# Optimization experiments

Measured on AMD Instinct MI355X. Metric: run time of the kernel, lower is better.

## Reference

```python
import jax, jax.numpy as jnp
import numpy as np

B, T, C, H = 2, 2048, 1024, 16  # batch, seq (== block_size), n_embd, n_head
HD = C // H  # head dim


def setup_inputs() -> dict:
    key = jax.random.key(0)
    k1, k2, k3 = jax.random.split(key, 3)
    x = jax.random.normal(k1, (B, T, C), dtype=jnp.float32)
    w_attn = jax.random.normal(k2, (C, 3 * C), dtype=jnp.float32) * (1.0 / np.sqrt(C))
    b_attn = jnp.zeros((3 * C,), dtype=jnp.float32)
    w_proj = jax.random.normal(k3, (C, C), dtype=jnp.float32) * (1.0 / np.sqrt(C))
    b_proj = jnp.zeros((C,), dtype=jnp.float32)
    return {"x": x, "w_attn": w_attn, "b_attn": b_attn, "w_proj": w_proj, "b_proj": b_proj}


def reference(x, w_attn, b_attn, w_proj, b_proj):
    # qkv projection: [B,T,3C]
    qkv = x @ w_attn + b_attn
    q, k, v = jnp.split(qkv, 3, axis=-1)
    # -> [B,H,T,HD]
    def to_heads(t):
        return t.reshape(B, T, H, HD).transpose(0, 2, 1, 3)
    q, k, v = to_heads(q), to_heads(k), to_heads(v)
    scale = 1.0 / np.sqrt(HD).astype(np.float32)
    # att: [B,H,T,T]
    att = jnp.einsum("bhqd,bhkd->bhqk", q, k) * scale
    causal = jnp.tril(jnp.ones((T, T), dtype=bool))
    att = jnp.where(causal[None, None], att, -jnp.inf)
    att = jax.nn.softmax(att, axis=-1)
    # y: [B,H,T,HD] -> [B,T,C]
    y = jnp.einsum("bhqk,bhkd->bhqd", att, v)
    y = y.transpose(0, 2, 1, 3).reshape(B, T, C)
    return y @ w_proj + b_proj
```

## Files before the change

kernel.cpp:

```cpp
#include <hip/hip_runtime.h>
#include <stdint.h>

#define Bb 2
#define Tt 2048
#define Cc 1024
#define Hh 16
#define HD 64
#define C3 3072

typedef __bf16 bf16x8 __attribute__((ext_vector_type(8)));
typedef float  f32x4  __attribute__((ext_vector_type(4)));
typedef unsigned short u16;
typedef u16 u16x8 __attribute__((ext_vector_type(8)));
typedef u16 u16x4 __attribute__((ext_vector_type(4)));

#define SCALE2 0.18033688f

__device__ __forceinline__ u16 f2bf(float f) {
  union { float f; unsigned u; } v; v.f = f;
  return (u16)((v.u + 0x7fffu + ((v.u >> 16) & 1u)) >> 16);
}
__device__ __forceinline__ u16 f2bf_fast(float f) {
  union { float f; unsigned u; } v; v.f = f;
  return (u16)((v.u + 0x8000u) >> 16);
}
__device__ __forceinline__ float bf2f(u16 a) {
  union { unsigned u; float f; } v; v.u = ((unsigned)a) << 16; return v.f;
}

__device__ __forceinline__ void gl2lds16(const void* g, void* s) {
  __builtin_amdgcn_global_load_lds(
      (__attribute__((address_space(1))) void*)(g),
      (__attribute__((address_space(3))) void*)(s), 16, 0, 0);
}

__device__ __forceinline__ bf16x8 ldb8(const u16* p) {
  return __builtin_bit_cast(bf16x8, *(const u16x8*)p);
}

__global__ __launch_bounds__(256)
void prep_kernel(const float* __restrict__ x, const float* __restrict__ w_attn,
                 const float* __restrict__ w_proj, u16* __restrict__ xb,
                 u16* __restrict__ wat, u16* __restrict__ wpt) {
  __shared__ u16 tile[64][65];
  const int blk = blockIdx.x;
  const int tid = threadIdx.x;
  if (blk < 4096) {
    int i = blk * 256 + tid;
    float4 v = ((const float4*)x)[i];
    u16x4 o = { f2bf(v.x), f2bf(v.y), f2bf(v.z), f2bf(v.w) };
    ((u16x4*)xb)[i] = o;
    return;
  }
  const float* in; u16* out; int R, C, c0, r0;
  if (blk < 4096 + 768) {
    int t = blk - 4096;
    in = w_attn; out = wat; R = 1024; C = 3072;
    c0 = (t % 48) * 64; r0 = (t / 48) * 64;
  } else {
    int t = blk - 4864;
    in = w_proj; out = wpt; R = 1024; C = 1024;
    c0 = (t & 15) * 64; r0 = (t >> 4) * 64;
  }
  int xx = tid & 63, yy = tid >> 6;
  #pragma unroll
  for (int rr = yy; rr < 64; rr += 4)
    tile[rr][xx] = f2bf(in[(size_t)(r0 + rr) * C + c0 + xx]);
  __syncthreads();
  #pragma unroll
  for (int rr = yy; rr < 64; rr += 4)
    out[(size_t)(c0 + rr) * R + r0 + xx] = tile[xx][rr];
}

template <int MODE, int BN>
__global__ __launch_bounds__(256, 4)
void gemm_bt(const u16* __restrict__ A, const u16* __restrict__ Bt,
             const float* __restrict__ bias, void* __restrict__ Cout,
             u16* __restrict__ Vt, int M, int N, int K) {
  __shared__ u16 As[2][128 * 32];
  __shared__ u16 Bs[2][BN * 32];
  constexpr int JT = BN / 32;
  const int tid = threadIdx.x;
  const int ln  = tid & 63;
  const int w   = tid >> 6;
  const int wm  = w >> 1, wn = w & 1;
  const int l15 = ln & 15, lq = ln >> 4;
  const int swz2 = (l15 >> 1) & 3;
  const int m0 = blockIdx.y * 128, n0 = blockIdx.x * BN;

  int aoff[2], boff[BN / 128 + 1];
  #pragma unroll
  for (int i = 0; i < 2; ++i) {
    int s = i * 256 + tid;
    int row = s >> 2, cg = (s & 3) ^ ((s >> 3) & 3);
    aoff[i] = (m0 + row) * K + cg * 8;
  }
  #pragma unroll
  for (int i = 0; i < BN / 128 + 1; ++i) {
    int s = i * 256 + tid;
    int row = s >> 2, cg = (s & 3) ^ ((s >> 3) & 3);
    boff[i] = (n0 + row) * K + cg * 8;
  }

  f32x4 acc[4][JT];
  #pragma unroll
  for (int i = 0; i < 4; ++i)
    #pragma unroll
    for (int j = 0; j < JT; ++j)
      acc[i][j] = (f32x4){0.f, 0.f, 0.f, 0.f};

  const int NK = K >> 5;
  #pragma unroll
  for (int i = 0; i < 2; ++i)
    gl2lds16(A + aoff[i], (char*)As[0] + (size_t)(i * 256 + w * 64) * 16);
  #pragma unroll
  for (int i = 0; i < BN / 128 + 1; ++i)
    gl2lds16(Bt + boff[i], (char*)Bs[0] + (size_t)(i * 256 + w * 64) * 16);

  for (int it = 0; it < NK; ++it) {
    const int p = it & 1;
    __syncthreads();
    if (it + 1 < NK) {
      const int k0 = (it + 1) * 32;
      #pragma unroll
      for (int i = 0; i < 2; ++i)
        gl2lds16(A + aoff[i] + k0, (char*)As[p ^ 1] + (size_t)(i * 256 + w * 64) * 16);
      #pragma unroll
      for (int i = 0; i < BN / 128 + 1; ++i)
        gl2lds16(Bt + boff[i] + k0, (char*)Bs[p ^ 1] + (size_t)(i * 256 + w * 64) * 16);
    }
    const u16* AsB = As[p];
    const u16* BsB = Bs[p];
    bf16x8 af[4], bfr[JT];
    #pragma unroll
    for (int i = 0; i < 4; ++i)
      af[i] = ldb8(&AsB[(wm * 64 + i * 16 + l15) * 32 + ((lq ^ swz2) * 8)]);
    #pragma unroll
    for (int j = 0; j < JT; ++j)
      bfr[j] = ldb8(&BsB[(wn * (BN / 2) + j * 16 + l15) * 32 + ((lq ^ swz2) * 8)]);
    #pragma unroll
    for (int i = 0; i < 4; ++i)
      #pragma unroll
      for (int j = 0; j < JT; ++j)
        acc[i][j] = __builtin_amdgcn_mfma_f32_16x16x32_bf16(af[i], bfr[j], acc[i][j], 0, 0, 0);
  }

  if (MODE == 1 && n0 >= 2048) {
    #pragma unroll
    for (int i = 0; i < 4; ++i) {
      int rowb = m0 + wm * 64 + i * 16 + lq * 4;
      int b_ = rowb >> 11, t0 = rowb & 2047;
      int tl = t0 & 63;
      int c = tl >> 4, ll = (tl >> 2) & 3;
      int pos0 = (c >> 1) * 32 + ll * 8 + (c & 1) * 4;
      size_t tdst = (size_t)(t0 & ~63) + pos0;
      #pragma unroll
      for (int j = 0; j < JT; ++j) {
        int col = n0 + wn * (BN / 2) + j * 16 + l15;
        int hd = col - 2048;
        float bsv = bias[col];
        u16x4 pk;
        #pragma unroll
        for (int r = 0; r < 4; ++r) pk[r] = f2bf(acc[i][j][r] + bsv);
        *(u16x4*)&Vt[(size_t)(b_ * 1024 + hd) * Tt + tdst] = pk;
      }
    }
  } else {
    const int ldc = (MODE == 1) ? 2048 : N;
    #pragma unroll
    for (int i = 0; i < 4; ++i) {
      int row = m0 + wm * 64 + i * 16 + lq * 4;
      #pragma unroll
      for (int j = 0; j < JT; ++j) {
        int col = n0 + wn * (BN / 2) + j * 16 + l15;
        float bsv = bias[col];
        #pragma unroll
        for (int r = 0; r < 4; ++r) {
          float v = acc[i][j][r] + bsv;
          if (MODE == 1) ((u16*)Cout)[(size_t)(row + r) * ldc + col] = f2bf(v);
          else           ((float*)Cout)[(size_t)(row + r) * ldc + col] = v;
        }
      }
    }
  }
}


__device__ __forceinline__ bf16x8 packp(const f32x4& a, const f32x4& b) {
  u16x8 u = { f2bf_fast(a[0]), f2bf_fast(a[1]), f2bf_fast(a[2]), f2bf_fast(a[3]),
              f2bf_fast(b[0]), f2bf_fast(b[1]), f2bf_fast(b[2]), f2bf_fast(b[3]) };
  return __builtin_bit_cast(bf16x8, u);
}
__device__ __forceinline__ bf16x8 qscale(const u16* p) {
  u16x8 q = *(const u16x8*)p;
  u16x8 s;
  #pragma unroll
  for (int j = 0; j < 8; ++j) s[j] = f2bf(bf2f(q[j]) * SCALE2);
  return __builtin_bit_cast(bf16x8, s);
}

__global__ __launch_bounds__(256, 4)
void attn_fused(const u16* __restrict__ qk, const u16* __restrict__ vt,
                u16* __restrict__ y) {
  __shared__ u16 Ks[2][64 * 64];
  __shared__ u16 Vts[2][64 * 64];
  const int tid = threadIdx.x;
  const int ln = tid & 63, w = tid >> 6;
  const int l15 = ln & 15, lq = ln >> 4;
  const int swz = l15 & 7;
  const int bx = blockIdx.x;
  const int bh = bx & 31;
  const int h  = bh & 15, b = bh >> 4;
  const int rr_ = bx >> 8, g = (bx >> 5) & 7;
  const int qt = (rr_ == 0) ? 31 - g : (rr_ == 1) ? 16 + g : (rr_ == 2) ? 15 - g : g;
  const int q0 = qt * 64;
  const int q0w = q0 + w * 16;

  const u16* qbase = qk + (size_t)(b * Tt) * 2048 + h * HD;
  const u16* kbase = qk + (size_t)(b * Tt) * 2048 + 1024 + h * HD;
  const u16* vbase = vt + (size_t)(b * 1024 + h * HD) * Tt;

  const int s0 = tid, s1 = 256 + tid;
  const int koff0 = (s0 >> 3) * 2048 + (((s0 & 7) ^ ((s0 >> 3) & 7)) * 8);
  const int koff1 = (s1 >> 3) * 2048 + (((s1 & 7) ^ ((s1 >> 3) & 7)) * 8);

  const u16* qrA = qbase + (size_t)(q0w + l15) * 2048;
  bf16x8 qA0 = qscale(qrA + lq * 8), qA1 = qscale(qrA + 32 + lq * 8);

  f32x4 o[4];
  #pragma unroll
  for (int j = 0; j < 4; ++j) o[j] = (f32x4){0,0,0,0};
  float m = -__builtin_inff(), l = 0.f;
  const int qg = q0w + l15;

  const int nkv = qt + 1;

  {
    gl2lds16(kbase + koff0, (char*)Ks[0] + w * 1024);
    gl2lds16(kbase + koff1, (char*)Ks[0] + 4096 + w * 1024);
    gl2lds16(vbase + koff0, (char*)Vts[0] + w * 1024);
    gl2lds16(vbase + koff1, (char*)Vts[0] + 4096 + w * 1024);
  }

  for (int it = 0; it < nkv; ++it) {
    const int kk = it * 64;
    const int p = it & 1;
    __syncthreads();
    if (it + 1 < nkv) {
      const u16* ksrc = kbase + (size_t)(kk + 64) * 2048;
      const u16* vsrc = vbase + kk + 64;
      gl2lds16(ksrc + koff0, (char*)Ks[p ^ 1] + w * 1024);
      gl2lds16(ksrc + koff1, (char*)Ks[p ^ 1] + 4096 + w * 1024);
      gl2lds16(vsrc + koff0, (char*)Vts[p ^ 1] + w * 1024);
      gl2lds16(vsrc + koff1, (char*)Vts[p ^ 1] + 4096 + w * 1024);
    }
    const u16* KsB  = Ks[p];
    const u16* VtsB = Vts[p];

    f32x4 t[4];
    #pragma unroll
    for (int i = 0; i < 4; ++i) t[i] = (f32x4){0,0,0,0};
    #pragma unroll
    for (int i = 0; i < 4; ++i) {
      bf16x8 kf0 = ldb8(&KsB[(i * 16 + l15) * 64 + ((lq    ) ^ swz) * 8]);
      bf16x8 kf1 = ldb8(&KsB[(i * 16 + l15) * 64 + ((lq + 4) ^ swz) * 8]);
      t[i] = __builtin_amdgcn_mfma_f32_16x16x32_bf16(kf0, qA0, t[i], 0, 0, 0);
      t[i] = __builtin_amdgcn_mfma_f32_16x16x32_bf16(kf1, qA1, t[i], 0, 0, 0);
    }

    const bool lastI = (it == nkv - 1);
    if (lastI) {
      #pragma unroll
      for (int i = 0; i < 4; ++i)
        #pragma unroll
        for (int r = 0; r < 4; ++r) {
          int kv = kk + i * 16 + lq * 4 + r;
          if (kv > qg) t[i][r] = -__builtin_inff();
        }
    }
    float mx = t[0][0];
    #pragma unroll
    for (int i = 0; i < 4; ++i)
      #pragma unroll
      for (int r = 0; r < 4; ++r) mx = fmaxf(mx, t[i][r]);
    mx = fmaxf(mx, __shfl_xor(mx, 16));
    mx = fmaxf(mx, __shfl_xor(mx, 32));
    float mn = fmaxf(m, mx);
    float al = __builtin_amdgcn_exp2f(m - mn);
    float ps = 0.f;
    #pragma unroll
    for (int i = 0; i < 4; ++i)
      #pragma unroll
      for (int r = 0; r < 4; ++r) {
        float pp = __builtin_amdgcn_exp2f(t[i][r] - mn);
        t[i][r] = pp;
        ps += pp;
      }
    ps += __shfl_xor(ps, 16);
    ps += __shfl_xor(ps, 32);
    l = l * al + ps;
    m = mn;
    #pragma unroll
    for (int jd = 0; jd < 4; ++jd)
      #pragma unroll
      for (int r = 0; r < 4; ++r) o[jd][r] *= al;

    bf16x8 p0 = packp(t[0], t[1]), p1 = packp(t[2], t[3]);
    #pragma unroll
    for (int mf = 0; mf < 2; ++mf) {
      bf16x8 pb = mf ? p1 : p0;
      #pragma unroll
      for (int jd = 0; jd < 4; ++jd) {
        int d = jd * 16 + l15;
        bf16x8 vf = ldb8(&VtsB[d * 64 + ((mf * 4 + lq) ^ swz) * 8]);
        o[jd] = __builtin_amdgcn_mfma_f32_16x16x32_bf16(vf, pb, o[jd], 0, 0, 0);
      }
    }
  }

  float inv = 1.f / l;
  const size_t ybase = (size_t)(b * Tt + q0w + l15) * Cc + h * HD;
  #pragma unroll
  for (int jd = 0; jd < 4; ++jd) {
    u16x4 pk;
    #pragma unroll
    for (int r = 0; r < 4; ++r) pk[r] = f2bf(o[jd][r] * inv);
    *(u16x4*)&y[ybase + jd * 16 + lq * 4] = pk;
  }
}

extern "C" void kernel_launch(void* const* d_in, const int* in_sizes, int n_in,
                              void* d_out, int out_size, void* d_ws, size_t ws_size,
                              hipStream_t stream) {
  const float* x      = (const float*)d_in[0];
  const float* w_attn = (const float*)d_in[1];
  const float* b_attn = (const float*)d_in[2];
  const float* w_proj = (const float*)d_in[3];
  const float* b_proj = (const float*)d_in[4];
  float* out = (float*)d_out;

  char* ws = (char*)d_ws;
  u16* xb  = (u16*)(ws + 0);
  u16* wat = (u16*)(ws + 8388608);
  u16* wpt = (u16*)(ws + 14680064);
  u16* qkb = (u16*)(ws + 16777216);
  u16* vtb = (u16*)(ws + 33554432);
  u16* yb  = (u16*)(ws + 41943040);

  prep_kernel<<<5120, 256, 0, stream>>>(x, w_attn, w_proj, xb, wat, wpt);
  gemm_bt<1, 128><<<dim3(24, 32), 256, 0, stream>>>(xb, wat, b_attn, (void*)qkb, vtb, 4096, 3072, 1024);
  attn_fused<<<1024, 256, 0, stream>>>(qkb, vtb, yb);
  gemm_bt<0, 64><<<dim3(16, 32), 256, 0, stream>>>(yb, wpt, b_proj, (void*)out, nullptr, 4096, 1024, 1024);
}
```

Baseline: 181.5 us.

## Pair complementary causal query tiles per block and add lazy softmax rescaling

Each attention block now processes two query tiles, qt and 31-qt, one after the other, so every block does the same number of KV iterations. Grid size drops from 1024 to 512, and the KV double buffer is prefetched across the boundary between the two tiles. The softmax rescale of the output accumulator is skipped unless the running max grows by more than a threshold, the P matrix is packed with native bf16 conversion, and the MFMA sections get raised wave priority. The trade-off is fewer blocks to hide latency, longer dependent work per block, and extra control flow.

```diff
diff --git a/kernel.cpp b/kernel.cpp
--- a/kernel.cpp
+++ b/kernel.cpp
@@ -19,10 +19,6 @@
 __device__ __forceinline__ u16 f2bf(float f) {
   union { float f; unsigned u; } v; v.f = f;
   return (u16)((v.u + 0x7fffu + ((v.u >> 16) & 1u)) >> 16);
-}
-__device__ __forceinline__ u16 f2bf_fast(float f) {
-  union { float f; unsigned u; } v; v.f = f;
-  return (u16)((v.u + 0x8000u) >> 16);
 }
 __device__ __forceinline__ float bf2f(u16 a) {
   union { unsigned u; float f; } v; v.u = ((unsigned)a) << 16; return v.f;
@@ -187,9 +183,10 @@
 
 
 __device__ __forceinline__ bf16x8 packp(const f32x4& a, const f32x4& b) {
-  u16x8 u = { f2bf_fast(a[0]), f2bf_fast(a[1]), f2bf_fast(a[2]), f2bf_fast(a[3]),
-              f2bf_fast(b[0]), f2bf_fast(b[1]), f2bf_fast(b[2]), f2bf_fast(b[3]) };
-  return __builtin_bit_cast(bf16x8, u);
+  bf16x8 r;
+  #pragma unroll
+  for (int i = 0; i < 4; ++i) { r[i] = (__bf16)a[i]; r[i + 4] = (__bf16)b[i]; }
+  return r;
 }
 __device__ __forceinline__ bf16x8 qscale(const u16* p) {
   u16x8 q = *(const u16x8*)p;
@@ -211,10 +208,7 @@
   const int bx = blockIdx.x;
   const int bh = bx & 31;
   const int h  = bh & 15, b = bh >> 4;
-  const int rr_ = bx >> 8, g = (bx >> 5) & 7;
-  const int qt = (rr_ == 0) ? 31 - g : (rr_ == 1) ? 16 + g : (rr_ == 2) ? 15 - g : g;
-  const int q0 = qt * 64;
-  const int q0w = q0 + w * 16;
+  const int pr = bx >> 5;
 
   const u16* qbase = qk + (size_t)(b * Tt) * 2048 + h * HD;
   const u16* kbase = qk + (size_t)(b * Tt) * 2048 + 1024 + h * HD;
@@ -224,108 +218,130 @@
   const int koff0 = (s0 >> 3) * 2048 + (((s0 & 7) ^ ((s0 >> 3) & 7)) * 8);
   const int koff1 = (s1 >> 3) * 2048 + (((s1 & 7) ^ ((s1 >> 3) & 7)) * 8);
 
-  const u16* qrA = qbase + (size_t)(q0w + l15) * 2048;
-  bf16x8 qA0 = qscale(qrA + lq * 8), qA1 = qscale(qrA + 32 + lq * 8);
-
-  f32x4 o[4];
-  #pragma unroll
-  for (int j = 0; j < 4; ++j) o[j] = (f32x4){0,0,0,0};
-  float m = -__builtin_inff(), l = 0.f;
-  const int qg = q0w + l15;
-
-  const int nkv = qt + 1;
-
-  {
-    gl2lds16(kbase + koff0, (char*)Ks[0] + w * 1024);
-    gl2lds16(kbase + koff1, (char*)Ks[0] + 4096 + w * 1024);
-    gl2lds16(vbase + koff0, (char*)Vts[0] + w * 1024);
-    gl2lds16(vbase + koff1, (char*)Vts[0] + 4096 + w * 1024);
-  }
-
-  for (int it = 0; it < nkv; ++it) {
-    const int kk = it * 64;
-    const int p = it & 1;
-    __syncthreads();
-    if (it + 1 < nkv) {
-      const u16* ksrc = kbase + (size_t)(kk + 64) * 2048;
-      const u16* vsrc = vbase + kk + 64;
-      gl2lds16(ksrc + koff0, (char*)Ks[p ^ 1] + w * 1024);
-      gl2lds16(ksrc + koff1, (char*)Ks[p ^ 1] + 4096 + w * 1024);
-      gl2lds16(vsrc + koff0, (char*)Vts[p ^ 1] + w * 1024);
-      gl2lds16(vsrc + koff1, (char*)Vts[p ^ 1] + 4096 + w * 1024);
-    }
-    const u16* KsB  = Ks[p];
-    const u16* VtsB = Vts[p];
-
-    f32x4 t[4];
-    #pragma unroll
-    for (int i = 0; i < 4; ++i) t[i] = (f32x4){0,0,0,0};
-    #pragma unroll
-    for (int i = 0; i < 4; ++i) {
-      bf16x8 kf0 = ldb8(&KsB[(i * 16 + l15) * 64 + ((lq    ) ^ swz) * 8]);
-      bf16x8 kf1 = ldb8(&KsB[(i * 16 + l15) * 64 + ((lq + 4) ^ swz) * 8]);
-      t[i] = __builtin_amdgcn_mfma_f32_16x16x32_bf16(kf0, qA0, t[i], 0, 0, 0);
-      t[i] = __builtin_amdgcn_mfma_f32_16x16x32_bf16(kf1, qA1, t[i], 0, 0, 0);
-    }
-
-    const bool lastI = (it == nkv - 1);
-    if (lastI) {
+  gl2lds16(kbase + koff0, (char*)Ks[0] + w * 1024);
+  gl2lds16(kbase + koff1, (char*)Ks[0] + 4096 + w * 1024);
+  gl2lds16(vbase + koff0, (char*)Vts[0] + w * 1024);
+  gl2lds16(vbase + koff1, (char*)Vts[0] + 4096 + w * 1024);
+
+  int pb = 0;
+
+  #pragma unroll
+  for (int half = 0; half < 2; ++half) {
+    const int qt = half ? pr : 31 - pr;
+    const int q0 = qt * 64;
+    const int q0w = q0 + w * 16;
+
+    const u16* qrA = qbase + (size_t)(q0w + l15) * 2048;
+    bf16x8 qA0 = qscale(qrA + lq * 8), qA1 = qscale(qrA + 32 + lq * 8);
+
+    f32x4 o[4];
+    #pragma unroll
+    for (int j = 0; j < 4; ++j) o[j] = (f32x4){0, 0, 0, 0};
+    float m = -__builtin_inff(), l = 0.f;
+    const int qg = q0w + l15;
+    const int nkv = qt + 1;
+
+    for (int it = 0; it < nkv; ++it) {
+      const int kk = it * 64;
+      const int p = pb ^ (it & 1);
+      __syncthreads();
+      if (it + 1 < nkv) {
+        const u16* ksrc = kbase + (size_t)(kk + 64) * 2048;
+        const u16* vsrc = vbase + kk + 64;
+        gl2lds16(ksrc + koff0, (char*)Ks[p ^ 1] + w * 1024);
+        gl2lds16(ksrc + koff1, (char*)Ks[p ^ 1] + 4096 + w * 1024);
+        gl2lds16(vsrc + koff0, (char*)Vts[p ^ 1] + w * 1024);
+        gl2lds16(vsrc + koff1, (char*)Vts[p ^ 1] + 4096 + w * 1024);
+      } else if (half == 0) {
+        gl2lds16(kbase + koff0, (char*)Ks[p ^ 1] + w * 1024);
+        gl2lds16(kbase + koff1, (char*)Ks[p ^ 1] + 4096 + w * 1024);
+        gl2lds16(vbase + koff0, (char*)Vts[p ^ 1] + w * 1024);
+        gl2lds16(vbase + koff1, (char*)Vts[p ^ 1] + 4096 + w * 1024);
+      }
+      const u16* KsB  = Ks[p];
+      const u16* VtsB = Vts[p];
+
+      f32x4 t[4];
+      #pragma unroll
+      for (int i = 0; i < 4; ++i) t[i] = (f32x4){0, 0, 0, 0};
+      __builtin_amdgcn_s_setprio(1);
+      #pragma unroll
+      for (int i = 0; i < 4; ++i) {
+        bf16x8 kf0 = ldb8(&KsB[(i * 16 + l15) * 64 + ((lq    ) ^ swz) * 8]);
+        bf16x8 kf1 = ldb8(&KsB[(i * 16 + l15) * 64 + ((lq + 4) ^ swz) * 8]);
+        t[i] = __builtin_amdgcn_mfma_f32_16x16x32_bf16(kf0, qA0, t[i], 0, 0, 0);
+        t[i] = __builtin_amdgcn_mfma_f32_16x16x32_bf16(kf1, qA1, t[i], 0, 0, 0);
+      }
+      __builtin_amdgcn_s_setprio(0);
+
+      if (it == nkv - 1) {
+        #pragma unroll
+        for (int i = 0; i < 4; ++i)
+          #pragma unroll
+          for (int r = 0; r < 4; ++r) {
+            int kv = kk + i * 16 + lq * 4 + r;
+            if (kv > qg) t[i][r] = -__builtin_inff();
+          }
+      }
+
+      float a0 = fmaxf(fmaxf(t[0][0], t[0][1]), fmaxf(t[0][2], t[0][3]));
+      float a1 = fmaxf(fmaxf(t[1][0], t[1][1]), fmaxf(t[1][2], t[1][3]));
+      float a2 = fmaxf(fmaxf(t[2][0], t[2][1]), fmaxf(t[2][2], t[2][3]));
+      float a3 = fmaxf(fmaxf(t[3][0], t[3][1]), fmaxf(t[3][2], t[3][3]));
+      float mx = fmaxf(fmaxf(a0, a1), fmaxf(a2, a3));
+      mx = fmaxf(mx, __shfl_xor(mx, 16));
+      mx = fmaxf(mx, __shfl_xor(mx, 32));
+
+      if (!__all(mx <= m + 8.0f)) {
+        float mn = fmaxf(m, mx);
+        float al = __builtin_amdgcn_exp2f(m - mn);
+        m = mn;
+        l *= al;
+        #pragma unroll
+        for (int jd = 0; jd < 4; ++jd)
+          #pragma unroll
+          for (int r = 0; r < 4; ++r) o[jd][r] *= al;
+      }
+
       #pragma unroll
       for (int i = 0; i < 4; ++i)
         #pragma unroll
-        for (int r = 0; r < 4; ++r) {
-          int kv = kk + i * 16 + lq * 4 + r;
-          if (kv > qg) t[i][r] = -__builtin_inff();
+        for (int r = 0; r < 4; ++r)
+          t[i][r] = __builtin_amdgcn_exp2f(t[i][r] - m);
+      float b0 = (t[0][0] + t[0][1]) + (t[0][2] + t[0][3]);
+      float b1 = (t[1][0] + t[1][1]) + (t[1][2] + t[1][3]);
+      float b2 = (t[2][0] + t[2][1]) + (t[2][2] + t[2][3]);
+      float b3 = (t[3][0] + t[3][1]) + (t[3][2] + t[3][3]);
+      float ps = (b0 + b1) + (b2 + b3);
+      ps += __shfl_xor(ps, 16);
+      ps += __shfl_xor(ps, 32);
+      l += ps;
+
+      bf16x8 p0 = packp(t[0], t[1]), p1 = packp(t[2], t[3]);
+      __builtin_amdgcn_s_setprio(1);
+      #pragma unroll
+      for (int mf = 0; mf < 2; ++mf) {
+        bf16x8 pbv = mf ? p1 : p0;
+        #pragma unroll
+        for (int jd = 0; jd < 4; ++jd) {
+          int d = jd * 16 + l15;
+          bf16x8 vf = ldb8(&VtsB[d * 64 + ((mf * 4 + lq) ^ swz) * 8]);
+          o[jd] = __builtin_amdgcn_mfma_f32_16x16x32_bf16(vf, pbv, o[jd], 0, 0, 0);
         }
-    }
-    float mx = t[0][0];
-    #pragma unroll
-    for (int i = 0; i < 4; ++i)
-      #pragma unroll
-      for (int r = 0; r < 4; ++r) mx = fmaxf(mx, t[i][r]);
-    mx = fmaxf(mx, __shfl_xor(mx, 16));
-    mx = fmaxf(mx, __shfl_xor(mx, 32));
-    float mn = fmaxf(m, mx);
-    float al = __builtin_amdgcn_exp2f(m - mn);
-    float ps = 0.f;
-    #pragma unroll
-    for (int i = 0; i < 4; ++i)
-      #pragma unroll
-      for (int r = 0; r < 4; ++r) {
-        float pp = __builtin_amdgcn_exp2f(t[i][r] - mn);
-        t[i][r] = pp;
-        ps += pp;
-      }
-    ps += __shfl_xor(ps, 16);
-    ps += __shfl_xor(ps, 32);
-    l = l * al + ps;
-    m = mn;
-    #pragma unroll
-    for (int jd = 0; jd < 4; ++jd)
-      #pragma unroll
-      for (int r = 0; r < 4; ++r) o[jd][r] *= al;
-
-    bf16x8 p0 = packp(t[0], t[1]), p1 = packp(t[2], t[3]);
-    #pragma unroll
-    for (int mf = 0; mf < 2; ++mf) {
-      bf16x8 pb = mf ? p1 : p0;
-      #pragma unroll
-      for (int jd = 0; jd < 4; ++jd) {
-        int d = jd * 16 + l15;
-        bf16x8 vf = ldb8(&VtsB[d * 64 + ((mf * 4 + lq) ^ swz) * 8]);
-        o[jd] = __builtin_amdgcn_mfma_f32_16x16x32_bf16(vf, pb, o[jd], 0, 0, 0);
-      }
-    }
-  }
-
-  float inv = 1.f / l;
-  const size_t ybase = (size_t)(b * Tt + q0w + l15) * Cc + h * HD;
-  #pragma unroll
-  for (int jd = 0; jd < 4; ++jd) {
-    u16x4 pk;
-    #pragma unroll
-    for (int r = 0; r < 4; ++r) pk[r] = f2bf(o[jd][r] * inv);
-    *(u16x4*)&y[ybase + jd * 16 + lq * 4] = pk;
+      }
+      __builtin_amdgcn_s_setprio(0);
+    }
+    pb ^= (nkv & 1);
+
+    float inv = 1.f / l;
+    const size_t ybase = (size_t)(b * Tt + q0w + l15) * Cc + h * HD;
+    #pragma unroll
+    for (int jd = 0; jd < 4; ++jd) {
+      u16x4 pk;
+      #pragma unroll
+      for (int r = 0; r < 4; ++r) pk[r] = f2bf(o[jd][r] * inv);
+      *(u16x4*)&y[ybase + jd * 16 + lq * 4] = pk;
+    }
   }
 }
 
@@ -349,6 +365,6 @@
 
   prep_kernel<<<5120, 256, 0, stream>>>(x, w_attn, w_proj, xb, wat, wpt);
   gemm_bt<1, 128><<<dim3(24, 32), 256, 0, stream>>>(xb, wat, b_attn, (void*)qkb, vtb, 4096, 3072, 1024);
-  attn_fused<<<1024, 256, 0, stream>>>(qkb, vtb, yb);
+  attn_fused<<<512, 256, 0, stream>>>(qkb, vtb, yb);
   gemm_bt<0, 64><<<dim3(16, 32), 256, 0, stream>>>(yb, wpt, b_proj, (void*)out, nullptr, 4096, 1024, 1024);
 }
```

New measurement: 176.4 us. -2.8%, faster.
